# Performance work log

Measured on AMD Instinct MI355X. Metric: run time of the kernel, lower is better.

The kernel has to match this reference:

```python
import jax, jax.numpy as jnp
import numpy as np


def mish(v):
    return v * jnp.tanh(jax.nn.softplus(v))


def setup_inputs() -> dict:
    key = jax.random.key(0)
    ks = jax.random.split(key, 10)
    B, C, W, H = 4, 256, 64, 64
    TAU, KV = 256, 512

    def wmat(k, shape, fan_in):
        return jax.random.normal(k, shape, jnp.float32) / np.float32(np.sqrt(fan_in))

    return {
        "x": jax.random.normal(ks[0], (B, C, W, H), jnp.float32),
        "y": jax.random.normal(ks[1], (B, TAU), jnp.float32),
        # ChannelProjBlock: 1x1 conv (weight-norm folded into effective weight) + Mish
        "Wp": wmat(ks[2], (C, C), C), "bp": jnp.zeros((C,), jnp.float32),
        # to_key_value MLP: Linear(tau, 2*kv) -> Mish -> Linear(2*kv, 2*kv)
        "W1": wmat(ks[3], (TAU, 2 * KV), TAU), "b1": jnp.zeros((2 * KV,), jnp.float32),
        "W2": wmat(ks[4], (2 * KV, 2 * KV), 2 * KV), "b2": jnp.zeros((2 * KV,), jnp.float32),
        # MultiheadAttention (1 head, kdim=vdim=KV): separate q/k/v/out projections
        "Wq": wmat(ks[5], (C, C), C), "bq": jnp.zeros((C,), jnp.float32),
        "Wk": wmat(ks[6], (KV, C), KV), "bk": jnp.zeros((C,), jnp.float32),
        "Wv": wmat(ks[7], (KV, C), KV), "bv": jnp.zeros((C,), jnp.float32),
        "Wo": wmat(ks[8], (C, C), C), "bo": jnp.zeros((C,), jnp.float32),
    }


def reference(x, y, Wp, bp, W1, b1, W2, b2, Wq, bq, Wk, bk, Wv, bv, Wo, bo):
    B, C, W, H = x.shape
    K = 3  # hardcoded kernel_size

    # ChannelProjBlock: 1x1 conv + Mish
    h0 = mish(jnp.einsum('bcwh,cd->bdwh', x, Wp) + bp[None, :, None, None])

    # nn.Unfold(kernel_size=3, stride=1, padding=1) -> [B, C*9, W*H]
    pad = jnp.pad(h0, ((0, 0), (0, 0), (1, 1), (1, 1)))
    # offset order matches torch unfold: (kh, kw) row-major, channel outermost
    patches = jnp.stack([pad[:, :, i:i + W, j:j + H]
                         for i in range(K) for j in range(K)], axis=2)  # [B,C,9,W,H]
    q = patches.reshape(B, C, K * K, W * H).transpose(0, 3, 2, 1)  # [B, WH, 9, C]

    # key/value from conditioning vector y
    kv = mish(y @ W1 + b1) @ W2 + b2            # [B, 2*KV]
    k_raw, v_raw = jnp.split(kv, 2, axis=-1)    # [B, KV] each (single KV token)

    # MultiheadAttention projections (1 head => head_dim = C)
    qp = q @ Wq + bq           # [B, WH, 9, C]
    kp = k_raw @ Wk + bk       # [B, C]
    vp = v_raw @ Wv + bv       # [B, C]

    scores = jnp.einsum('bpqc,bc->bpq', qp, kp) / jnp.sqrt(jnp.asarray(C, x.dtype))
    attw = jax.nn.softmax(scores[..., None], axis=-1)  # key len 1 -> all ones
    att = attw * vp[:, None, None, :]                  # [B, WH, 9, C]
    o = att @ Wo + bo                                  # out_proj

    # view -> permute -> sum over the 9 kernel positions -> [B, C, W, H]
    out = o.sum(axis=2).transpose(0, 2, 1).reshape(B, C, W, H)
    return out
```

## Files before the change

### kernel.cpp

```cpp
#include <hip/hip_runtime.h>


__device__ __forceinline__ float mishf(float v) {
    float sp = (v > 20.0f) ? v : log1pf(expf(v));
    return v * tanhf(sp);
}

__global__ __launch_bounds__(256) void k_hidden(const float* __restrict__ y,
                                                const float* __restrict__ W1,
                                                const float* __restrict__ b1,
                                                float* __restrict__ hidden) {
    int b  = blockIdx.x >> 6;
    int j0 = (blockIdx.x & 63) * 16;
    int t  = threadIdx.x;
    int col = j0 + (t & 15);
    int kc  = t >> 4;
    __shared__ float y_s[256];
    __shared__ float ps[256];
    y_s[t] = y[b * 256 + t];
    __syncthreads();
    const float* w  = W1 + (size_t)(kc * 16) * 1024 + col;
    const float* ys = y_s + kc * 16;
    float a0 = 0, a1 = 0, a2 = 0, a3 = 0;
    #pragma unroll
    for (int r = 0; r < 16; r += 4) {
        a0 = fmaf(ys[r + 0], w[(r + 0) * 1024], a0);
        a1 = fmaf(ys[r + 1], w[(r + 1) * 1024], a1);
        a2 = fmaf(ys[r + 2], w[(r + 2) * 1024], a2);
        a3 = fmaf(ys[r + 3], w[(r + 3) * 1024], a3);
    }
    ps[t] = (a0 + a1) + (a2 + a3);
    __syncthreads();
    if (t < 16) {
        float s = 0;
        #pragma unroll
        for (int k = 0; k < 16; ++k) s += ps[t + 16 * k];
        hidden[b * 1024 + j0 + t] = mishf(s + b1[j0 + t]);
    }
}

__global__ __launch_bounds__(256) void k_vraw_vppart(const float* __restrict__ hidden,
                                                     const float* __restrict__ W2,
                                                     const float* __restrict__ b2,
                                                     const float* __restrict__ Wv,
                                                     float* __restrict__ vp_part) {
    int b  = blockIdx.x >> 5;
    int c0 = (blockIdx.x & 31) * 16;
    int t  = threadIdx.x;
    int col = c0 + (t & 15);
    int kc  = t >> 4;
    __shared__ float4 h4_s[256];
    __shared__ float ps[256];
    __shared__ float vr16[16];
    h4_s[t] = ((const float4*)(hidden + b * 1024))[t];
    __syncthreads();
    const float* h_s = (const float*)h4_s;
    const float* w  = W2 + (size_t)(kc * 64) * 1024 + 512 + col;
    const float* hs = h_s + kc * 64;
    float a0 = 0, a1 = 0, a2 = 0, a3 = 0;
    for (int r = 0; r < 64; r += 4) {
        a0 = fmaf(hs[r + 0], w[(size_t)(r + 0) * 1024], a0);
        a1 = fmaf(hs[r + 1], w[(size_t)(r + 1) * 1024], a1);
        a2 = fmaf(hs[r + 2], w[(size_t)(r + 2) * 1024], a2);
        a3 = fmaf(hs[r + 3], w[(size_t)(r + 3) * 1024], a3);
    }
    ps[t] = (a0 + a1) + (a2 + a3);
    __syncthreads();
    if (t < 16) {
        float s = 0;
        #pragma unroll
        for (int k = 0; k < 16; ++k) s += ps[t + 16 * k];
        vr16[t] = s + b2[512 + c0 + t];
    }
    __syncthreads();
    const float* wv = Wv + (size_t)c0 * 256 + t;
    float acc0 = 0, acc1 = 0;
    #pragma unroll
    for (int k = 0; k < 16; k += 2) {
        acc0 = fmaf(vr16[k],     wv[(k + 0) * 256], acc0);
        acc1 = fmaf(vr16[k + 1], wv[(k + 1) * 256], acc1);
    }
    vp_part[(size_t)blockIdx.x * 256 + t] = acc0 + acc1;
}

__global__ __launch_bounds__(256) void k_out3(const float* __restrict__ vp_part,
                                              const float* __restrict__ bv,
                                              const float* __restrict__ Wo,
                                              const float* __restrict__ bo,
                                              float4* __restrict__ out) {
    int b = blockIdx.x >> 8, c = blockIdx.x & 255, t = threadIdx.x;
    __shared__ float red[256];
    float wo = Wo[(size_t)t * 256 + c];
    const float* vpp = vp_part + (size_t)b * 32 * 256 + t;
    float s0 = 0, s1 = 0, s2 = 0, s3 = 0;
    #pragma unroll
    for (int p = 0; p < 32; p += 4) {
        s0 += vpp[(p + 0) * 256];
        s1 += vpp[(p + 1) * 256];
        s2 += vpp[(p + 2) * 256];
        s3 += vpp[(p + 3) * 256];
    }
    float vpv = ((s0 + s1) + (s2 + s3)) + bv[t];
    red[t] = vpv * wo;
    __syncthreads();
    int l = t & 63;
    float s = (red[l] + red[l + 64]) + (red[l + 128] + red[l + 192]);
    s += __shfl_xor(s, 32);
    s += __shfl_xor(s, 16);
    s += __shfl_xor(s, 8);
    s += __shfl_xor(s, 4);
    s += __shfl_xor(s, 2);
    s += __shfl_xor(s, 1);
    float v = 9.0f * (s + bo[c]);
    float4 vv = make_float4(v, v, v, v);
    float4* p = out + (size_t)blockIdx.x * 1024;
    p[t]       = vv;
    p[t + 256] = vv;
    p[t + 512] = vv;
    p[t + 768] = vv;
}

__global__ __launch_bounds__(256) void k_vraw(const float* __restrict__ hidden,
                                              const float* __restrict__ W2,
                                              const float* __restrict__ b2,
                                              float* __restrict__ v_raw) {
    int b  = blockIdx.x >> 5;
    int c0 = (blockIdx.x & 31) * 16;
    int t  = threadIdx.x;
    int col = c0 + (t & 15);
    int kc  = t >> 4;
    __shared__ float h_s[1024];
    __shared__ float ps[256];
    h_s[t]       = hidden[b * 1024 + t];
    h_s[t + 256] = hidden[b * 1024 + t + 256];
    h_s[t + 512] = hidden[b * 1024 + t + 512];
    h_s[t + 768] = hidden[b * 1024 + t + 768];
    __syncthreads();
    const float* w  = W2 + (size_t)(kc * 64) * 1024 + 512 + col;
    const float* hs = h_s + kc * 64;
    float a0 = 0, a1 = 0, a2 = 0, a3 = 0;
    for (int r = 0; r < 64; r += 4) {
        a0 = fmaf(hs[r + 0], w[(size_t)(r + 0) * 1024], a0);
        a1 = fmaf(hs[r + 1], w[(size_t)(r + 1) * 1024], a1);
        a2 = fmaf(hs[r + 2], w[(size_t)(r + 2) * 1024], a2);
        a3 = fmaf(hs[r + 3], w[(size_t)(r + 3) * 1024], a3);
    }
    ps[t] = (a0 + a1) + (a2 + a3);
    __syncthreads();
    if (t < 16) {
        float s = 0;
        #pragma unroll
        for (int k = 0; k < 16; ++k) s += ps[t + 16 * k];
        v_raw[b * 512 + c0 + t] = s + b2[512 + c0 + t];
    }
}

__global__ __launch_bounds__(256) void k_vp(const float* __restrict__ v_raw,
                                            const float* __restrict__ Wv,
                                            const float* __restrict__ bv,
                                            float* __restrict__ vp) {
    int b  = blockIdx.x >> 3;
    int d0 = (blockIdx.x & 7) * 32;
    int t  = threadIdx.x;
    int col = d0 + (t & 31), kc = t >> 5;
    __shared__ float v_s[512];
    __shared__ float ps[256];
    v_s[t]       = v_raw[b * 512 + t];
    v_s[t + 256] = v_raw[b * 512 + t + 256];
    __syncthreads();
    const float* w  = Wv + (size_t)(kc * 64) * 256 + col;
    const float* vs = v_s + kc * 64;
    float a0 = 0, a1 = 0, a2 = 0, a3 = 0;
    for (int r = 0; r < 64; r += 4) {
        a0 = fmaf(vs[r + 0], w[(r + 0) * 256], a0);
        a1 = fmaf(vs[r + 1], w[(r + 1) * 256], a1);
        a2 = fmaf(vs[r + 2], w[(r + 2) * 256], a2);
        a3 = fmaf(vs[r + 3], w[(r + 3) * 256], a3);
    }
    ps[t] = (a0 + a1) + (a2 + a3);
    __syncthreads();
    if (t < 32) {
        float s = 0;
        #pragma unroll
        for (int k = 0; k < 8; ++k) s += ps[t + 32 * k];
        vp[b * 256 + d0 + t] = s + bv[d0 + t];
    }
}

__global__ __launch_bounds__(256) void k_out(const float* __restrict__ vp,
                                             const float* __restrict__ Wo,
                                             const float* __restrict__ bo,
                                             float4* __restrict__ out) {
    int b = blockIdx.x >> 8, c = blockIdx.x & 255, t = threadIdx.x;
    __shared__ float red[256];
    red[t] = vp[b * 256 + t] * Wo[(size_t)t * 256 + c];
    __syncthreads();
    if (t < 64) {
        float s = (red[t] + red[t + 64]) + (red[t + 128] + red[t + 192]);
        s += __shfl_down(s, 32);
        s += __shfl_down(s, 16);
        s += __shfl_down(s, 8);
        s += __shfl_down(s, 4);
        s += __shfl_down(s, 2);
        s += __shfl_down(s, 1);
        if (t == 0) red[0] = 9.0f * (s + bo[c]);
    }
    __syncthreads();
    float v = red[0];
    float4 vv = make_float4(v, v, v, v);
    float4* p = out + (size_t)blockIdx.x * 1024;
    p[t]       = vv;
    p[t + 256] = vv;
    p[t + 512] = vv;
    p[t + 768] = vv;
}

extern "C" void kernel_launch(void* const* d_in, const int* in_sizes, int n_in,
                              void* d_out, int out_size, void* d_ws, size_t ws_size,
                              hipStream_t stream) {
    const float* y  = (const float*)d_in[1];
    const float* W1 = (const float*)d_in[4];
    const float* b1 = (const float*)d_in[5];
    const float* W2 = (const float*)d_in[6];
    const float* b2 = (const float*)d_in[7];
    const float* Wv = (const float*)d_in[12];
    const float* bv = (const float*)d_in[13];
    const float* Wo = (const float*)d_in[14];
    const float* bo = (const float*)d_in[15];

    float* ws      = (float*)d_ws;
    float* hidden  = ws;
    float* vp_part = ws + 4096;
    const size_t need = (size_t)(4096 + 32768) * 4;

    if (ws_size >= need) {
        k_hidden     <<<256,  256, 0, stream>>>(y, W1, b1, hidden);
        k_vraw_vppart<<<128,  256, 0, stream>>>(hidden, W2, b2, Wv, vp_part);
        k_out3       <<<1024, 256, 0, stream>>>(vp_part, bv, Wo, bo, (float4*)d_out);
    } else {
        float* v_raw = ws + 4096;
        float* vp    = ws + 6144;
        k_hidden<<<256,  256, 0, stream>>>(y, W1, b1, hidden);
        k_vraw  <<<128,  256, 0, stream>>>(hidden, W2, b2, v_raw);
        k_vp    <<<32,   256, 0, stream>>>(v_raw, Wv, bv, vp);
        k_out   <<<1024, 256, 0, stream>>>(vp, Wo, bo, (float4*)d_out);
    }
}
```

Baseline: 20.05 us.

## Push Wo projection into partial-sum kernel and precompute bias vector

The output projection through Wo is now applied to each per-block partial of vp inside the second kernel, producing partial output values that already include the factor of 9. The bias term (bv·Wo + bo)·9 is computed by an extra block in the first kernel. The final kernel becomes a pure reduction of 32 partials plus a broadcast, written with nontemporal stores. This takes the Wo gather and block reduction out of the 1024-block broadcast kernel, at the cost of each of the 128 blocks in kernel two reading all of Wo.

```diff
diff --git a/kernel.cpp b/kernel.cpp
--- a/kernel.cpp
+++ b/kernel.cpp
@@ -1,49 +1,71 @@
 #include <hip/hip_runtime.h>
 
+
+typedef float floatx4 __attribute__((ext_vector_type(4)));
 
 __device__ __forceinline__ float mishf(float v) {
     float sp = (v > 20.0f) ? v : log1pf(expf(v));
     return v * tanhf(sp);
 }
 
-__global__ __launch_bounds__(256) void k_hidden(const float* __restrict__ y,
-                                                const float* __restrict__ W1,
-                                                const float* __restrict__ b1,
-                                                float* __restrict__ hidden) {
-    int b  = blockIdx.x >> 6;
-    int j0 = (blockIdx.x & 63) * 16;
-    int t  = threadIdx.x;
-    int col = j0 + (t & 15);
-    int kc  = t >> 4;
-    __shared__ float y_s[256];
-    __shared__ float ps[256];
-    y_s[t] = y[b * 256 + t];
-    __syncthreads();
-    const float* w  = W1 + (size_t)(kc * 16) * 1024 + col;
-    const float* ys = y_s + kc * 16;
-    float a0 = 0, a1 = 0, a2 = 0, a3 = 0;
-    #pragma unroll
-    for (int r = 0; r < 16; r += 4) {
-        a0 = fmaf(ys[r + 0], w[(r + 0) * 1024], a0);
-        a1 = fmaf(ys[r + 1], w[(r + 1) * 1024], a1);
-        a2 = fmaf(ys[r + 2], w[(r + 2) * 1024], a2);
-        a3 = fmaf(ys[r + 3], w[(r + 3) * 1024], a3);
-    }
-    ps[t] = (a0 + a1) + (a2 + a3);
-    __syncthreads();
-    if (t < 16) {
-        float s = 0;
-        #pragma unroll
-        for (int k = 0; k < 16; ++k) s += ps[t + 16 * k];
-        hidden[b * 1024 + j0 + t] = mishf(s + b1[j0 + t]);
-    }
-}
-
-__global__ __launch_bounds__(256) void k_vraw_vppart(const float* __restrict__ hidden,
-                                                     const float* __restrict__ W2,
-                                                     const float* __restrict__ b2,
-                                                     const float* __restrict__ Wv,
-                                                     float* __restrict__ vp_part) {
+__global__ __launch_bounds__(256) void k1_hidden_cvec(const float* __restrict__ y,
+                                                      const float* __restrict__ W1,
+                                                      const float* __restrict__ b1,
+                                                      const float* __restrict__ bv,
+                                                      const float* __restrict__ Wo,
+                                                      const float* __restrict__ bo,
+                                                      float* __restrict__ hidden,
+                                                      float* __restrict__ cvec) {
+    int t = threadIdx.x;
+    __shared__ float s_in[256];
+    __shared__ float ps[256];
+    if (blockIdx.x < 256) {
+        int b  = blockIdx.x >> 6;
+        int j0 = (blockIdx.x & 63) * 16;
+        int col = j0 + (t & 15);
+        int kc  = t >> 4;
+        s_in[t] = y[b * 256 + t];
+        __syncthreads();
+        const float* w  = W1 + (size_t)(kc * 16) * 1024 + col;
+        const float* ys = s_in + kc * 16;
+        float a0 = 0, a1 = 0, a2 = 0, a3 = 0;
+        #pragma unroll
+        for (int r = 0; r < 16; r += 4) {
+            a0 = fmaf(ys[r + 0], w[(r + 0) * 1024], a0);
+            a1 = fmaf(ys[r + 1], w[(r + 1) * 1024], a1);
+            a2 = fmaf(ys[r + 2], w[(r + 2) * 1024], a2);
+            a3 = fmaf(ys[r + 3], w[(r + 3) * 1024], a3);
+        }
+        ps[t] = (a0 + a1) + (a2 + a3);
+        __syncthreads();
+        if (t < 16) {
+            float s = 0;
+            #pragma unroll
+            for (int k = 0; k < 16; ++k) s += ps[t + 16 * k];
+            hidden[b * 1024 + j0 + t] = mishf(s + b1[j0 + t]);
+        }
+    } else {
+        s_in[t] = bv[t];
+        __syncthreads();
+        const float* w = Wo + t;
+        float a0 = 0, a1 = 0, a2 = 0, a3 = 0;
+        #pragma unroll 4
+        for (int d = 0; d < 256; d += 4) {
+            a0 = fmaf(s_in[d + 0], w[(d + 0) * 256], a0);
+            a1 = fmaf(s_in[d + 1], w[(d + 1) * 256], a1);
+            a2 = fmaf(s_in[d + 2], w[(d + 2) * 256], a2);
+            a3 = fmaf(s_in[d + 3], w[(d + 3) * 256], a3);
+        }
+        cvec[t] = 9.0f * (((a0 + a1) + (a2 + a3)) + bo[t]);
+    }
+}
+
+__global__ __launch_bounds__(256) void k2_vraw_o9part(const float* __restrict__ hidden,
+                                                      const float* __restrict__ W2,
+                                                      const float* __restrict__ b2,
+                                                      const float* __restrict__ Wv,
+                                                      const float* __restrict__ Wo,
+                                                      float* __restrict__ o9part) {
     int b  = blockIdx.x >> 5;
     int c0 = (blockIdx.x & 31) * 16;
     int t  = threadIdx.x;
@@ -80,50 +102,72 @@
         acc0 = fmaf(vr16[k],     wv[(k + 0) * 256], acc0);
         acc1 = fmaf(vr16[k + 1], wv[(k + 1) * 256], acc1);
     }
-    vp_part[(size_t)blockIdx.x * 256 + t] = acc0 + acc1;
-}
-
-__global__ __launch_bounds__(256) void k_out3(const float* __restrict__ vp_part,
-                                              const float* __restrict__ bv,
-                                              const float* __restrict__ Wo,
-                                              const float* __restrict__ bo,
-                                              float4* __restrict__ out) {
+    ps[t] = acc0 + acc1;
+    __syncthreads();
+    const float* wo = Wo + t;
+    float o0 = 0, o1 = 0, o2 = 0, o3 = 0;
+    #pragma unroll 4
+    for (int d = 0; d < 256; d += 4) {
+        o0 = fmaf(ps[d + 0], wo[(d + 0) * 256], o0);
+        o1 = fmaf(ps[d + 1], wo[(d + 1) * 256], o1);
+        o2 = fmaf(ps[d + 2], wo[(d + 2) * 256], o2);
+        o3 = fmaf(ps[d + 3], wo[(d + 3) * 256], o3);
+    }
+    o9part[(size_t)blockIdx.x * 256 + t] = 9.0f * ((o0 + o1) + (o2 + o3));
+}
+
+__global__ __launch_bounds__(256) void k3_bcast(const float* __restrict__ o9part,
+                                                const float* __restrict__ cvec,
+                                                floatx4* __restrict__ out) {
     int b = blockIdx.x >> 8, c = blockIdx.x & 255, t = threadIdx.x;
-    __shared__ float red[256];
-    float wo = Wo[(size_t)t * 256 + c];
-    const float* vpp = vp_part + (size_t)b * 32 * 256 + t;
-    float s0 = 0, s1 = 0, s2 = 0, s3 = 0;
-    #pragma unroll
-    for (int p = 0; p < 32; p += 4) {
-        s0 += vpp[(p + 0) * 256];
-        s1 += vpp[(p + 1) * 256];
-        s2 += vpp[(p + 2) * 256];
-        s3 += vpp[(p + 3) * 256];
-    }
-    float vpv = ((s0 + s1) + (s2 + s3)) + bv[t];
-    red[t] = vpv * wo;
-    __syncthreads();
-    int l = t & 63;
-    float s = (red[l] + red[l + 64]) + (red[l + 128] + red[l + 192]);
-    s += __shfl_xor(s, 32);
-    s += __shfl_xor(s, 16);
-    s += __shfl_xor(s, 8);
-    s += __shfl_xor(s, 4);
-    s += __shfl_xor(s, 2);
-    s += __shfl_xor(s, 1);
-    float v = 9.0f * (s + bo[c]);
-    float4 vv = make_float4(v, v, v, v);
-    float4* p = out + (size_t)blockIdx.x * 1024;
-    p[t]       = vv;
-    p[t + 256] = vv;
-    p[t + 512] = vv;
-    p[t + 768] = vv;
-}
-
-__global__ __launch_bounds__(256) void k_vraw(const float* __restrict__ hidden,
-                                              const float* __restrict__ W2,
-                                              const float* __restrict__ b2,
-                                              float* __restrict__ v_raw) {
+    float v = o9part[(size_t)(b * 32 + (t & 31)) * 256 + c];
+    v += __shfl_xor(v, 16);
+    v += __shfl_xor(v, 8);
+    v += __shfl_xor(v, 4);
+    v += __shfl_xor(v, 2);
+    v += __shfl_xor(v, 1);
+    v += cvec[c];
+    floatx4 vv = {v, v, v, v};
+    floatx4* p = out + (size_t)blockIdx.x * 1024;
+    __builtin_nontemporal_store(vv, &p[t]);
+    __builtin_nontemporal_store(vv, &p[t + 256]);
+    __builtin_nontemporal_store(vv, &p[t + 512]);
+    __builtin_nontemporal_store(vv, &p[t + 768]);
+}
+
+__global__ __launch_bounds__(256) void k_hidden_fb(const float* __restrict__ y,
+                                                   const float* __restrict__ W1,
+                                                   const float* __restrict__ b1,
+                                                   float* __restrict__ hidden) {
+    int b  = blockIdx.x >> 4;
+    int j0 = (blockIdx.x & 15) * 64;
+    int t  = threadIdx.x;
+    int col = j0 + (t & 63);
+    int kc  = t >> 6;
+    __shared__ float y_s[256];
+    __shared__ float ps[256];
+    y_s[t] = y[b * 256 + t];
+    __syncthreads();
+    const float* w  = W1 + (size_t)(kc * 64) * 1024 + col;
+    const float* ys = y_s + kc * 64;
+    float a0 = 0, a1 = 0, a2 = 0, a3 = 0;
+    for (int r = 0; r < 64; r += 4) {
+        a0 = fmaf(ys[r + 0], w[(r + 0) * 1024], a0);
+        a1 = fmaf(ys[r + 1], w[(r + 1) * 1024], a1);
+        a2 = fmaf(ys[r + 2], w[(r + 2) * 1024], a2);
+        a3 = fmaf(ys[r + 3], w[(r + 3) * 1024], a3);
+    }
+    ps[t] = (a0 + a1) + (a2 + a3);
+    __syncthreads();
+    if (t < 64)
+        hidden[b * 1024 + j0 + t] =
+            mishf((ps[t] + ps[t + 64]) + (ps[t + 128] + ps[t + 192]) + b1[j0 + t]);
+}
+
+__global__ __launch_bounds__(256) void k_vraw_fb(const float* __restrict__ hidden,
+                                                 const float* __restrict__ W2,
+                                                 const float* __restrict__ b2,
+                                                 float* __restrict__ v_raw) {
     int b  = blockIdx.x >> 5;
     int c0 = (blockIdx.x & 31) * 16;
     int t  = threadIdx.x;
@@ -155,10 +199,10 @@
     }
 }
 
-__global__ __launch_bounds__(256) void k_vp(const float* __restrict__ v_raw,
-                                            const float* __restrict__ Wv,
-                                            const float* __restrict__ bv,
-                                            float* __restrict__ vp) {
+__global__ __launch_bounds__(256) void k_vp_fb(const float* __restrict__ v_raw,
+                                               const float* __restrict__ Wv,
+                                               const float* __restrict__ bv,
+                                               float* __restrict__ vp) {
     int b  = blockIdx.x >> 3;
     int d0 = (blockIdx.x & 7) * 32;
     int t  = threadIdx.x;
@@ -187,10 +231,10 @@
     }
 }
 
-__global__ __launch_bounds__(256) void k_out(const float* __restrict__ vp,
-                                             const float* __restrict__ Wo,
-                                             const float* __restrict__ bo,
-                                             float4* __restrict__ out) {
+__global__ __launch_bounds__(256) void k_out_fb(const float* __restrict__ vp,
+                                                const float* __restrict__ Wo,
+                                                const float* __restrict__ bo,
+                                                float4* __restrict__ out) {
     int b = blockIdx.x >> 8, c = blockIdx.x & 255, t = threadIdx.x;
     __shared__ float red[256];
     red[t] = vp[b * 256 + t] * Wo[(size_t)t * 256 + c];
@@ -228,21 +272,22 @@
     const float* Wo = (const float*)d_in[14];
     const float* bo = (const float*)d_in[15];
 
-    float* ws      = (float*)d_ws;
-    float* hidden  = ws;
-    float* vp_part = ws + 4096;
-    const size_t need = (size_t)(4096 + 32768) * 4;
+    float* ws     = (float*)d_ws;
+    float* hidden = ws;
+    float* o9part = ws + 4096;
+    float* cvec   = ws + 4096 + 32768;
+    const size_t need = (size_t)(4096 + 32768 + 256) * 4;
 
     if (ws_size >= need) {
-        k_hidden     <<<256,  256, 0, stream>>>(y, W1, b1, hidden);
-        k_vraw_vppart<<<128,  256, 0, stream>>>(hidden, W2, b2, Wv, vp_part);
-        k_out3       <<<1024, 256, 0, stream>>>(vp_part, bv, Wo, bo, (float4*)d_out);
+        k1_hidden_cvec<<<257,  256, 0, stream>>>(y, W1, b1, bv, Wo, bo, hidden, cvec);
+        k2_vraw_o9part<<<128,  256, 0, stream>>>(hidden, W2, b2, Wv, Wo, o9part);
+        k3_bcast      <<<1024, 256, 0, stream>>>(o9part, cvec, (floatx4*)d_out);
     } else {
         float* v_raw = ws + 4096;
         float* vp    = ws + 6144;
-        k_hidden<<<256,  256, 0, stream>>>(y, W1, b1, hidden);
-        k_vraw  <<<128,  256, 0, stream>>>(hidden, W2, b2, v_raw);
-        k_vp    <<<32,   256, 0, stream>>>(v_raw, Wv, bv, vp);
-        k_out   <<<1024, 256, 0, stream>>>(vp, Wo, bo, (float4*)d_out);
-    }
-}
+        k_hidden_fb<<<64,   256, 0, stream>>>(y, W1, b1, hidden);
+        k_vraw_fb  <<<128,  256, 0, stream>>>(hidden, W2, b2, v_raw);
+        k_vp_fb    <<<32,   256, 0, stream>>>(v_raw, Wv, bv, vp);
+        k_out_fb   <<<1024, 256, 0, stream>>>(vp, Wo, bo, (float4*)d_out);
+    }
+}
```

Result: slower. 21.20 us (+5.7%).
